# Optimization experiments

Hardware: AMD Instinct MI355X
Metric: run time of the kernel (lower is better)

The kernel has to match this reference:

```python
import jax, jax.numpy as jnp
import numpy as np
from jax import lax

DIM = 8        # per-head dim
HEADS = 32     # inp // dim
EPS = 1e-15    # linear-attention eps
BN_EPS = 1e-5  # torch BatchNorm2d default eps


def _conv(x, w, groups=1, pad=0):
    return lax.conv_general_dilated(
        x, w, window_strides=(1, 1), padding=[(pad, pad), (pad, pad)],
        feature_group_count=groups,
        dimension_numbers=('NCHW', 'OIHW', 'NCHW'))


def setup_inputs() -> dict:
    key = jax.random.key(0)
    ks = jax.random.split(key, 9)
    B, C, H, W = 8, 256, 64, 64
    td = HEADS * DIM  # 256
    x = jax.random.normal(ks[0], (B, C, H, W), jnp.float32)
    w_qkv = jax.random.normal(ks[1], (3 * td, C, 1, 1), jnp.float32) * 0.05
    w_dw = jax.random.normal(ks[2], (3 * td, 1, 5, 5), jnp.float32) * 0.05
    w_pw = jax.random.normal(ks[3], (3 * td, (3 * td) // (3 * HEADS), 1, 1), jnp.float32) * 0.05
    w_proj = jax.random.normal(ks[4], (C, 2 * td, 1, 1), jnp.float32) * 0.05
    bn_gamma = 1.0 + 0.1 * jax.random.normal(ks[5], (C,), jnp.float32)
    bn_beta = 0.1 * jax.random.normal(ks[6], (C,), jnp.float32)
    bn_mean = 0.1 * jax.random.normal(ks[7], (C,), jnp.float32)
    bn_var = jnp.ones((C,), jnp.float32)
    return dict(x=x, w_qkv=w_qkv, w_dw=w_dw, w_pw=w_pw, w_proj=w_proj,
                bn_gamma=bn_gamma, bn_beta=bn_beta, bn_mean=bn_mean, bn_var=bn_var)


def reference(x, w_qkv, w_dw, w_pw, w_proj, bn_gamma, bn_beta, bn_mean, bn_var):
    B, _, H, W = x.shape
    # qkv: 1x1 conv, no bias/norm/act
    qkv = _conv(x, w_qkv)                                   # (B, 3*td, H, W)
    # aggreg branch: depthwise 5x5 then grouped 1x1 (groups = 3*heads)
    agg = _conv(qkv, w_dw, groups=w_dw.shape[0], pad=2)
    agg = _conv(agg, w_pw, groups=3 * HEADS)
    ms = jnp.concatenate([qkv, agg], axis=1)                # (B, 2*3*td, H, W)
    # relu linear attention
    G = ms.shape[1] // (3 * DIM)                            # 2*heads = 64
    t = ms.reshape(B, G, 3 * DIM, H * W).transpose(0, 1, 3, 2)  # (B, G, N, 3d)
    q = jax.nn.relu(t[..., :DIM])
    k = jax.nn.relu(t[..., DIM:2 * DIM])
    v = t[..., 2 * DIM:]
    v = jnp.pad(v, ((0, 0), (0, 0), (0, 0), (0, 1)), constant_values=1.0)  # ones trick
    kv = jnp.einsum('bgnd,bgne->bgde', k, v)                # (B, G, d, d+1)
    out = jnp.einsum('bgnd,bgde->bgne', q, kv)              # (B, G, N, d+1)
    out = out[..., :-1] / (out[..., -1:] + EPS)
    out = out.transpose(0, 1, 3, 2).reshape(B, G * DIM, H, W)  # (B, 2*td, H, W)
    # proj: 1x1 conv + BatchNorm2d (eval mode), no act
    out = _conv(out, w_proj)
    inv = jax.lax.rsqrt(bn_var + BN_EPS)
    out = (out - bn_mean[:, None, None]) * (inv * bn_gamma)[:, None, None] + bn_beta[:, None, None]
    return out
```

## Files before the change

### kernel.cpp

```cpp
#include <hip/hip_runtime.h>

#define NPIX 4096

__global__ __launch_bounds__(256) void sgemm(
    const float* __restrict__ A,
    const float* __restrict__ Bm,
    float* __restrict__ C,
    int M, int K,
    const float* __restrict__ bn_g, const float* __restrict__ bn_b,
    const float* __restrict__ bn_m, const float* __restrict__ bn_v)
{
    __shared__ float As[16][128];
    __shared__ float Bs[16][128];

    const int tid = threadIdx.x;
    const int tx  = tid & 15;
    const int ty  = tid >> 4;
    const int n0  = blockIdx.x * 128;
    const int m0  = blockIdx.y * 128;
    const int bz  = blockIdx.z;

    const float* __restrict__ Bp = Bm + (size_t)bz * K * NPIX;

    const int ar = tid >> 1;
    const int ac = (tid & 1) * 8;
    const int bk = tid >> 4;
    const int bn4 = (tid & 15) * 4;

    float acc[8][8] = {};

    for (int k0 = 0; k0 < K; k0 += 16) {
        const float* ap = A + (size_t)(m0 + ar) * K + k0 + ac;
        float4 ga0 = *(const float4*)(ap);
        float4 ga1 = *(const float4*)(ap + 4);
        const float* bp = Bp + (size_t)(k0 + bk) * NPIX + n0 + bn4;
        float4 gb0 = *(const float4*)(bp);
        float4 gb1 = *(const float4*)(bp + 64);

        __syncthreads();

        As[ac + 0][ar] = ga0.x;
        As[ac + 1][ar] = ga0.y;
        As[ac + 2][ar] = ga0.z;
        As[ac + 3][ar] = ga0.w;
        As[ac + 4][ar] = ga1.x;
        As[ac + 5][ar] = ga1.y;
        As[ac + 6][ar] = ga1.z;
        As[ac + 7][ar] = ga1.w;
        *(float4*)&Bs[bk][bn4]      = gb0;
        *(float4*)&Bs[bk][bn4 + 64] = gb1;

        __syncthreads();

#pragma unroll
        for (int kk = 0; kk < 16; ++kk) {
            float av[8], bv[8];
            *(float4*)&av[0] = *(const float4*)&As[kk][ty * 8];
            *(float4*)&av[4] = *(const float4*)&As[kk][ty * 8 + 4];
            *(float4*)&bv[0] = *(const float4*)&Bs[kk][tx * 4];
            *(float4*)&bv[4] = *(const float4*)&Bs[kk][tx * 4 + 64];
#pragma unroll
            for (int i = 0; i < 8; ++i)
#pragma unroll
                for (int j = 0; j < 8; ++j)
                    acc[i][j] = fmaf(av[i], bv[j], acc[i][j]);
        }
    }

    float* __restrict__ Cp = C + (size_t)bz * M * NPIX;
#pragma unroll
    for (int i = 0; i < 8; ++i) {
        const int m = m0 + ty * 8 + i;
        float sc = 1.0f, off = 0.0f;
        if (bn_g) {
            sc  = (1.0f / sqrtf(bn_v[m] + 1e-5f)) * bn_g[m];
            off = bn_b[m] - bn_m[m] * sc;
        }
        float4 v0, v1;
        v0.x = acc[i][0] * sc + off;  v0.y = acc[i][1] * sc + off;
        v0.z = acc[i][2] * sc + off;  v0.w = acc[i][3] * sc + off;
        v1.x = acc[i][4] * sc + off;  v1.y = acc[i][5] * sc + off;
        v1.z = acc[i][6] * sc + off;  v1.w = acc[i][7] * sc + off;
        *(float4*)(Cp + (size_t)m * NPIX + n0 + tx * 4)      = v0;
        *(float4*)(Cp + (size_t)m * NPIX + n0 + 64 + tx * 4) = v1;
    }
}

__global__ __launch_bounds__(256) void dwpw(
    const float* __restrict__ qkv,
    const float* __restrict__ w_dw,
    const float* __restrict__ w_pw,
    float* __restrict__ agg)
{
    __shared__ float sm[8][20][20];
    __shared__ float wdw[8][25];
    __shared__ float wpw[8][8];

    const int tid = threadIdx.x;
    const int p   = blockIdx.z % 96;
    const int b   = blockIdx.z / 96;
    const int y0  = blockIdx.y * 16;
    const int x0  = blockIdx.x * 16;

    const float* __restrict__ src = qkv + ((size_t)b * 768 + 8 * p) * NPIX;

    for (int i = tid; i < 8 * 400; i += 256) {
        int c = i / 400, r = i % 400;
        int sy = r / 20, sx = r % 20;
        int gy = y0 + sy - 2, gx = x0 + sx - 2;
        float v = 0.0f;
        if ((unsigned)gy < 64u && (unsigned)gx < 64u)
            v = src[(size_t)c * NPIX + gy * 64 + gx];
        sm[c][sy][sx] = v;
    }
    if (tid < 200) {
        int c = tid / 25, t = tid % 25;
        wdw[c][t] = w_dw[(size_t)(8 * p + c) * 25 + t];
    }
    if (tid < 64) {
        int o = tid / 8, i = tid % 8;
        wpw[o][i] = w_pw[(size_t)(8 * p + o) * 8 + i];
    }
    __syncthreads();

    const int ty = tid >> 4, tx = tid & 15;

    float d[8];
#pragma unroll
    for (int c = 0; c < 8; ++c) {
        float s = 0.0f;
#pragma unroll
        for (int ky = 0; ky < 5; ++ky)
#pragma unroll
            for (int kx = 0; kx < 5; ++kx)
                s += wdw[c][ky * 5 + kx] * sm[c][ty + ky][tx + kx];
        d[c] = s;
    }

    float* __restrict__ dst = agg + ((size_t)b * 768 + 8 * p) * NPIX + (y0 + ty) * 64 + (x0 + tx);
#pragma unroll
    for (int o = 0; o < 8; ++o) {
        float s = 0.0f;
#pragma unroll
        for (int i = 0; i < 8; ++i) s += wpw[o][i] * d[i];
        dst[(size_t)o * NPIX] = s;
    }
}

__global__ __launch_bounds__(256) void kv_reduce(
    const float* __restrict__ qkv, const float* __restrict__ agg,
    float* __restrict__ kvb)
{
    const int g = blockIdx.x, b = blockIdx.y;
    const float* __restrict__ src = (g < 32) ? qkv : agg;
    const float* __restrict__ base = src + ((size_t)b * 768 + 24 * (g & 31)) * NPIX;

    float acc[72];
#pragma unroll
    for (int i = 0; i < 72; ++i) acc[i] = 0.0f;

    for (int n = threadIdx.x; n < NPIX; n += 256) {
        float kf[8], vf[8];
#pragma unroll
        for (int d = 0; d < 8; ++d) kf[d] = fmaxf(0.0f, base[(size_t)(8 + d) * NPIX + n]);
#pragma unroll
        for (int e = 0; e < 8; ++e) vf[e] = base[(size_t)(16 + e) * NPIX + n];
#pragma unroll
        for (int d = 0; d < 8; ++d) {
#pragma unroll
            for (int e = 0; e < 8; ++e) acc[d * 9 + e] += kf[d] * vf[e];
            acc[d * 9 + 8] += kf[d];
        }
    }

    const int lane = threadIdx.x & 63;
    const int wv   = threadIdx.x >> 6;
#pragma unroll
    for (int i = 0; i < 72; ++i) {
        float v = acc[i];
        v += __shfl_xor(v, 32, 64);
        v += __shfl_xor(v, 16, 64);
        v += __shfl_xor(v, 8, 64);
        v += __shfl_xor(v, 4, 64);
        v += __shfl_xor(v, 2, 64);
        v += __shfl_xor(v, 1, 64);
        acc[i] = v;
    }
    __shared__ float red[4][72];
    if (lane == 0) {
#pragma unroll
        for (int i = 0; i < 72; ++i) red[wv][i] = acc[i];
    }
    __syncthreads();
    if (threadIdx.x < 72)
        kvb[((size_t)b * 64 + g) * 72 + threadIdx.x] =
            red[0][threadIdx.x] + red[1][threadIdx.x] +
            red[2][threadIdx.x] + red[3][threadIdx.x];
}

__global__ __launch_bounds__(256) void attn_apply(
    const float* __restrict__ qkv, const float* __restrict__ agg,
    const float* __restrict__ kvb,
    float* __restrict__ att)
{
    const int g = blockIdx.y, b = blockIdx.z;
    const int n = blockIdx.x * 256 + threadIdx.x;

    __shared__ float kvs[72];
    if (threadIdx.x < 72) kvs[threadIdx.x] = kvb[((size_t)b * 64 + g) * 72 + threadIdx.x];
    __syncthreads();

    const float* __restrict__ src = (g < 32) ? qkv : agg;
    const float* __restrict__ base = src + ((size_t)b * 768 + 24 * (g & 31)) * NPIX;

    float q[8];
#pragma unroll
    for (int d = 0; d < 8; ++d) q[d] = fmaxf(0.0f, base[(size_t)d * NPIX + n]);

    float o[9] = {};
#pragma unroll
    for (int d = 0; d < 8; ++d) {
        float qd = q[d];
#pragma unroll
        for (int e = 0; e < 9; ++e) o[e] += qd * kvs[d * 9 + e];
    }
    float den = o[8] + 1e-15f;

    float* __restrict__ dst = att + ((size_t)b * 512 + g * 8) * NPIX + n;
#pragma unroll
    for (int e = 0; e < 8; ++e) dst[(size_t)e * NPIX] = o[e] / den;
}

extern "C" void kernel_launch(void* const* d_in, const int* in_sizes, int n_in,
                              void* d_out, int out_size, void* d_ws, size_t ws_size,
                              hipStream_t stream) {
    const float* x      = (const float*)d_in[0];
    const float* w_qkv  = (const float*)d_in[1];
    const float* w_dw   = (const float*)d_in[2];
    const float* w_pw   = (const float*)d_in[3];
    const float* w_proj = (const float*)d_in[4];
    const float* bn_g   = (const float*)d_in[5];
    const float* bn_b   = (const float*)d_in[6];
    const float* bn_m   = (const float*)d_in[7];
    const float* bn_v   = (const float*)d_in[8];
    float* out = (float*)d_out;

    char* ws = (char*)d_ws;
    float* qkv = (float*)ws;
    float* agg = (float*)(ws + 100663296ull);
    float* att = (float*)(ws + 201326592ull);
    float* kvb = (float*)d_out;

    sgemm<<<dim3(32, 6, 8), dim3(256), 0, stream>>>(
        w_qkv, x, qkv, 768, 256, nullptr, nullptr, nullptr, nullptr);

    dwpw<<<dim3(4, 4, 8 * 96), dim3(256), 0, stream>>>(qkv, w_dw, w_pw, agg);

    kv_reduce<<<dim3(64, 8), dim3(256), 0, stream>>>(qkv, agg, kvb);

    attn_apply<<<dim3(16, 64, 8), dim3(256), 0, stream>>>(qkv, agg, kvb, att);

    sgemm<<<dim3(32, 2, 8), dim3(256), 0, stream>>>(
        w_proj, att, out, 256, 512, bn_g, bn_b, bn_m, bn_v);
}
```

Baseline: 497.4 us.

## Run qkv 1x1 conv on bf16 MFMA with 3-way split, vectorize attention kernels

Replaces the fp32 SIMT GEMM for the qkv projection with a bf16 MFMA kernel. Both operands are split into high/mid/low bf16 parts and six cross products are accumulated to keep close to fp32 accuracy. A new pre-pass transposes x into pixel-major bf16 triplets, reusing the attention workspace buffer. kv_reduce and attn_apply are also changed to process four pixels per thread with float4 loads and stores. The cost is an extra transpose/split kernel, extra memory traffic, and six MFMA passes instead of one.

Result: no change. 488.1 us (-1.9%).

```diff
diff --git a/kernel.cpp b/kernel.cpp
--- a/kernel.cpp
+++ b/kernel.cpp
@@ -1,6 +1,165 @@
 #include <hip/hip_runtime.h>
 
+typedef __bf16 bf16;
+typedef __bf16 bf16x4 __attribute__((ext_vector_type(4)));
+typedef __bf16 bf16x8 __attribute__((ext_vector_type(8)));
+typedef float f32x4 __attribute__((ext_vector_type(4)));
+
 #define NPIX 4096
+
+__global__ __launch_bounds__(256) void split_x(
+    const float* __restrict__ x,
+    bf16* __restrict__ xTh, bf16* __restrict__ xTm, bf16* __restrict__ xTl)
+{
+    const int pix = blockIdx.x * 256 + threadIdx.x;
+    const int k0  = blockIdx.y * 32;
+    const int b   = blockIdx.z;
+
+    const float* __restrict__ src = x + ((size_t)b * 256 + k0) * NPIX + pix;
+    float v[32];
+#pragma unroll
+    for (int kk = 0; kk < 32; ++kk) v[kk] = src[(size_t)kk * NPIX];
+
+    const size_t drow = ((size_t)b * NPIX + pix) * 256 + k0;
+#pragma unroll
+    for (int c = 0; c < 4; ++c) {
+        bf16x8 vh, vm, vl;
+#pragma unroll
+        for (int j = 0; j < 8; ++j) {
+            float val = v[c * 8 + j];
+            bf16 h = (bf16)val; float r  = val - (float)h;
+            bf16 m = (bf16)r;   float r2 = r - (float)m;
+            vh[j] = h; vm[j] = m; vl[j] = (bf16)r2;
+        }
+        *(bf16x8*)(xTh + drow + c * 8) = vh;
+        *(bf16x8*)(xTm + drow + c * 8) = vm;
+        *(bf16x8*)(xTl + drow + c * 8) = vl;
+    }
+}
+
+__global__ __launch_bounds__(256, 2) void qkv_mfma(
+    const float* __restrict__ A,
+    const bf16* __restrict__ xTh,
+    const bf16* __restrict__ xTm,
+    const bf16* __restrict__ xTl,
+    float* __restrict__ C)
+{
+    __shared__ bf16 As[3][128][40];
+
+    const int tid  = threadIdx.x;
+    const int lane = tid & 63;
+    const int wv   = tid >> 6;
+    const int col  = lane & 15;
+    const int quad = lane >> 4;
+    const int wm   = (wv >> 1) * 64;
+    const int wn   = (wv & 1) * 64;
+    const int n0   = blockIdx.x * 128;
+    const int m0   = blockIdx.y * 128;
+    const int b    = blockIdx.z;
+
+    const int arow = tid >> 1;
+    const int akc  = (tid & 1) * 16;
+
+    const size_t xoff = ((size_t)b * NPIX + n0 + wn) * 256;
+
+    f32x4 acc[4][4] = {};
+
+    float av[16];
+    {
+        const float* ap = A + (size_t)(m0 + arow) * 256 + akc;
+        *(float4*)&av[0]  = *(const float4*)(ap);
+        *(float4*)&av[4]  = *(const float4*)(ap + 4);
+        *(float4*)&av[8]  = *(const float4*)(ap + 8);
+        *(float4*)&av[12] = *(const float4*)(ap + 12);
+    }
+
+    for (int k0 = 0; k0 < 256; k0 += 32) {
+        __syncthreads();
+
+#pragma unroll
+        for (int c = 0; c < 4; ++c) {
+            bf16x4 vh, vm, vl;
+#pragma unroll
+            for (int j = 0; j < 4; ++j) {
+                float val = av[c * 4 + j];
+                bf16 h = (bf16)val; float r  = val - (float)h;
+                bf16 m = (bf16)r;   float r2 = r - (float)m;
+                vh[j] = h; vm[j] = m; vl[j] = (bf16)r2;
+            }
+            *(bf16x4*)&As[0][arow][akc + c * 4] = vh;
+            *(bf16x4*)&As[1][arow][akc + c * 4] = vm;
+            *(bf16x4*)&As[2][arow][akc + c * 4] = vl;
+        }
+
+        if (k0 + 32 < 256) {
+            const float* ap = A + (size_t)(m0 + arow) * 256 + k0 + 32 + akc;
+            *(float4*)&av[0]  = *(const float4*)(ap);
+            *(float4*)&av[4]  = *(const float4*)(ap + 4);
+            *(float4*)&av[8]  = *(const float4*)(ap + 8);
+            *(float4*)&av[12] = *(const float4*)(ap + 12);
+        }
+
+        __syncthreads();
+
+        bf16x8 bh[4], bm[4], bl[4];
+#pragma unroll
+        for (int t = 0; t < 4; ++t) {
+            const size_t brow = xoff + (size_t)(t * 16 + col) * 256 + k0 + quad * 8;
+            bh[t] = *(const bf16x8*)(xTh + brow);
+            bm[t] = *(const bf16x8*)(xTm + brow);
+            bl[t] = *(const bf16x8*)(xTl + brow);
+        }
+        bf16x8 af[4][3];
+#pragma unroll
+        for (int s = 0; s < 4; ++s)
+#pragma unroll
+            for (int p = 0; p < 3; ++p)
+                af[s][p] = *(const bf16x8*)&As[p][wm + s * 16 + col][quad * 8];
+
+#pragma unroll
+        for (int t = 0; t < 4; ++t)
+#pragma unroll
+            for (int s = 0; s < 4; ++s)
+                acc[s][t] = __builtin_amdgcn_mfma_f32_16x16x32_bf16(af[s][2], bh[t], acc[s][t], 0, 0, 0);
+#pragma unroll
+        for (int t = 0; t < 4; ++t)
+#pragma unroll
+            for (int s = 0; s < 4; ++s)
+                acc[s][t] = __builtin_amdgcn_mfma_f32_16x16x32_bf16(af[s][0], bl[t], acc[s][t], 0, 0, 0);
+#pragma unroll
+        for (int t = 0; t < 4; ++t)
+#pragma unroll
+            for (int s = 0; s < 4; ++s)
+                acc[s][t] = __builtin_amdgcn_mfma_f32_16x16x32_bf16(af[s][1], bm[t], acc[s][t], 0, 0, 0);
+#pragma unroll
+        for (int t = 0; t < 4; ++t)
+#pragma unroll
+            for (int s = 0; s < 4; ++s)
+                acc[s][t] = __builtin_amdgcn_mfma_f32_16x16x32_bf16(af[s][1], bh[t], acc[s][t], 0, 0, 0);
+#pragma unroll
+        for (int t = 0; t < 4; ++t)
+#pragma unroll
+            for (int s = 0; s < 4; ++s)
+                acc[s][t] = __builtin_amdgcn_mfma_f32_16x16x32_bf16(af[s][0], bm[t], acc[s][t], 0, 0, 0);
+#pragma unroll
+        for (int t = 0; t < 4; ++t)
+#pragma unroll
+            for (int s = 0; s < 4; ++s)
+                acc[s][t] = __builtin_amdgcn_mfma_f32_16x16x32_bf16(af[s][0], bh[t], acc[s][t], 0, 0, 0);
+    }
+
+    float* __restrict__ Cp = C + (size_t)b * 768 * NPIX;
+#pragma unroll
+    for (int s = 0; s < 4; ++s)
+#pragma unroll
+        for (int t = 0; t < 4; ++t)
+#pragma unroll
+            for (int r = 0; r < 4; ++r) {
+                const int m = m0 + wm + s * 16 + quad * 4 + r;
+                const int n = n0 + wn + t * 16 + col;
+                Cp[(size_t)m * NPIX + n] = acc[s][t][r];
+            }
+}
 
 __global__ __launch_bounds__(256) void sgemm(
     const float* __restrict__ A,
@@ -39,14 +198,10 @@
 
         __syncthreads();
 
-        As[ac + 0][ar] = ga0.x;
-        As[ac + 1][ar] = ga0.y;
-        As[ac + 2][ar] = ga0.z;
-        As[ac + 3][ar] = ga0.w;
-        As[ac + 4][ar] = ga1.x;
-        As[ac + 5][ar] = ga1.y;
-        As[ac + 6][ar] = ga1.z;
-        As[ac + 7][ar] = ga1.w;
+        As[ac + 0][ar] = ga0.x;  As[ac + 1][ar] = ga0.y;
+        As[ac + 2][ar] = ga0.z;  As[ac + 3][ar] = ga0.w;
+        As[ac + 4][ar] = ga1.x;  As[ac + 5][ar] = ga1.y;
+        As[ac + 6][ar] = ga1.z;  As[ac + 7][ar] = ga1.w;
         *(float4*)&Bs[bk][bn4]      = gb0;
         *(float4*)&Bs[bk][bn4 + 64] = gb1;
 
@@ -54,16 +209,16 @@
 
 #pragma unroll
         for (int kk = 0; kk < 16; ++kk) {
-            float av[8], bv[8];
-            *(float4*)&av[0] = *(const float4*)&As[kk][ty * 8];
-            *(float4*)&av[4] = *(const float4*)&As[kk][ty * 8 + 4];
-            *(float4*)&bv[0] = *(const float4*)&Bs[kk][tx * 4];
-            *(float4*)&bv[4] = *(const float4*)&Bs[kk][tx * 4 + 64];
+            float avv[8], bvv[8];
+            *(float4*)&avv[0] = *(const float4*)&As[kk][ty * 8];
+            *(float4*)&avv[4] = *(const float4*)&As[kk][ty * 8 + 4];
+            *(float4*)&bvv[0] = *(const float4*)&Bs[kk][tx * 4];
+            *(float4*)&bvv[4] = *(const float4*)&Bs[kk][tx * 4 + 64];
 #pragma unroll
             for (int i = 0; i < 8; ++i)
 #pragma unroll
                 for (int j = 0; j < 8; ++j)
-                    acc[i][j] = fmaf(av[i], bv[j], acc[i][j]);
+                    acc[i][j] = fmaf(avv[i], bvv[j], acc[i][j]);
         }
     }
 
@@ -159,17 +314,24 @@
 #pragma unroll
     for (int i = 0; i < 72; ++i) acc[i] = 0.0f;
 
-    for (int n = threadIdx.x; n < NPIX; n += 256) {
-        float kf[8], vf[8];
-#pragma unroll
-        for (int d = 0; d < 8; ++d) kf[d] = fmaxf(0.0f, base[(size_t)(8 + d) * NPIX + n]);
-#pragma unroll
-        for (int e = 0; e < 8; ++e) vf[e] = base[(size_t)(16 + e) * NPIX + n];
+    for (int i4 = threadIdx.x; i4 < NPIX / 4; i4 += 256) {
+        float4 kf[8], vf[8];
 #pragma unroll
         for (int d = 0; d < 8; ++d) {
-#pragma unroll
-            for (int e = 0; e < 8; ++e) acc[d * 9 + e] += kf[d] * vf[e];
-            acc[d * 9 + 8] += kf[d];
+            float4 t = ((const float4*)(base + (size_t)(8 + d) * NPIX))[i4];
+            kf[d].x = fmaxf(0.0f, t.x); kf[d].y = fmaxf(0.0f, t.y);
+            kf[d].z = fmaxf(0.0f, t.z); kf[d].w = fmaxf(0.0f, t.w);
+        }
+#pragma unroll
+        for (int e = 0; e < 8; ++e)
+            vf[e] = ((const float4*)(base + (size_t)(16 + e) * NPIX))[i4];
+#pragma unroll
+        for (int d = 0; d < 8; ++d) {
+#pragma unroll
+            for (int e = 0; e < 8; ++e)
+                acc[d * 9 + e] += kf[d].x * vf[e].x + kf[d].y * vf[e].y +
+                                  kf[d].z * vf[e].z + kf[d].w * vf[e].w;
+            acc[d * 9 + 8] += kf[d].x + kf[d].y + kf[d].z + kf[d].w;
         }
     }
 
@@ -204,7 +366,7 @@
     float* __restrict__ att)
 {
     const int g = blockIdx.y, b = blockIdx.z;
-    const int n = blockIdx.x * 256 + threadIdx.x;
+    const int n4 = blockIdx.x * 256 + threadIdx.x;
 
     __shared__ float kvs[72];
     if (threadIdx.x < 72) kvs[threadIdx.x] = kvb[((size_t)b * 64 + g) * 72 + threadIdx.x];
@@ -213,22 +375,36 @@
     const float* __restrict__ src = (g < 32) ? qkv : agg;
     const float* __restrict__ base = src + ((size_t)b * 768 + 24 * (g & 31)) * NPIX;
 
-    float q[8];
-#pragma unroll
-    for (int d = 0; d < 8; ++d) q[d] = fmaxf(0.0f, base[(size_t)d * NPIX + n]);
-
-    float o[9] = {};
+    float4 q[8];
 #pragma unroll
     for (int d = 0; d < 8; ++d) {
-        float qd = q[d];
-#pragma unroll
-        for (int e = 0; e < 9; ++e) o[e] += qd * kvs[d * 9 + e];
-    }
-    float den = o[8] + 1e-15f;
-
-    float* __restrict__ dst = att + ((size_t)b * 512 + g * 8) * NPIX + n;
-#pragma unroll
-    for (int e = 0; e < 8; ++e) dst[(size_t)e * NPIX] = o[e] / den;
+        float4 t = ((const float4*)(base + (size_t)d * NPIX))[n4];
+        q[d].x = fmaxf(0.0f, t.x); q[d].y = fmaxf(0.0f, t.y);
+        q[d].z = fmaxf(0.0f, t.z); q[d].w = fmaxf(0.0f, t.w);
+    }
+
+    float4 o[9];
+#pragma unroll
+    for (int e = 0; e < 9; ++e) { o[e].x = 0; o[e].y = 0; o[e].z = 0; o[e].w = 0; }
+#pragma unroll
+    for (int d = 0; d < 8; ++d)
+#pragma unroll
+        for (int e = 0; e < 9; ++e) {
+            float w = kvs[d * 9 + e];
+            o[e].x += q[d].x * w; o[e].y += q[d].y * w;
+            o[e].z += q[d].z * w; o[e].w += q[d].w * w;
+        }
+    float dx = o[8].x + 1e-15f, dy = o[8].y + 1e-15f;
+    float dz = o[8].z + 1e-15f, dw = o[8].w + 1e-15f;
+
+    float* __restrict__ dst = att + ((size_t)b * 512 + g * 8) * NPIX;
+#pragma unroll
+    for (int e = 0; e < 8; ++e) {
+        float4 r;
+        r.x = o[e].x / dx; r.y = o[e].y / dy;
+        r.z = o[e].z / dz; r.w = o[e].w / dw;
+        ((float4*)(dst + (size_t)e * NPIX))[n4] = r;
+    }
 }
 
 extern "C" void kernel_launch(void* const* d_in, const int* in_sizes, int n_in,
@@ -248,17 +424,22 @@
     char* ws = (char*)d_ws;
     float* qkv = (float*)ws;
     float* agg = (float*)(ws + 100663296ull);
-    float* att = (float*)(ws + 201326592ull);
+    char*  attc = ws + 201326592ull;
+    float* att = (float*)attc;
+    bf16*  xTh = (bf16*)attc;
+    bf16*  xTm = (bf16*)(attc + 16777216ull);
+    bf16*  xTl = (bf16*)(attc + 33554432ull);
     float* kvb = (float*)d_out;
 
-    sgemm<<<dim3(32, 6, 8), dim3(256), 0, stream>>>(
-        w_qkv, x, qkv, 768, 256, nullptr, nullptr, nullptr, nullptr);
+    split_x<<<dim3(16, 8, 8), dim3(256), 0, stream>>>(x, xTh, xTm, xTl);
+
+    qkv_mfma<<<dim3(32, 6, 8), dim3(256), 0, stream>>>(w_qkv, xTh, xTm, xTl, qkv);
 
     dwpw<<<dim3(4, 4, 8 * 96), dim3(256), 0, stream>>>(qkv, w_dw, w_pw, agg);
 
     kv_reduce<<<dim3(64, 8), dim3(256), 0, stream>>>(qkv, agg, kvb);
 
-    attn_apply<<<dim3(16, 64, 8), dim3(256), 0, stream>>>(qkv, agg, kvb, att);
+    attn_apply<<<dim3(4, 64, 8), dim3(256), 0, stream>>>(qkv, agg, kvb, att);
 
     sgemm<<<dim3(32, 2, 8), dim3(256), 0, stream>>>(
         w_proj, att, out, 256, 512, bn_g, bn_b, bn_m, bn_v);
```
